# Optimization experiments

Measured on AMD Instinct MI355X. Metric: run time of the kernel, lower is better.

The kernel has to match this reference:

```python
import jax, jax.numpy as jnp
import numpy as np

B, S, D, H = 2, 2048, 1024, 16
DH = D // H  # per-head dim = 64


def setup_inputs() -> dict:
    key = jax.random.key(0)
    k0, k1, k2, k3, k4, k5 = jax.random.split(key, 6)
    x = jax.random.normal(k0, (B, S, D), dtype=jnp.float32)
    # mask: True where token is valid, False where padded ([B, S, 1] bool)
    mask = jax.random.randint(k1, (B, S, 1), 0, 2).astype(bool)
    scale = 0.02
    # Per-head projection weights stacked over heads: [H, D, DH]
    Wq = jax.random.normal(k2, (H, D, DH), dtype=jnp.float32) * scale
    Wk = jax.random.normal(k3, (H, D, DH), dtype=jnp.float32) * scale
    Wv = jax.random.normal(k4, (H, D, DH), dtype=jnp.float32) * scale
    # Output projection, torch Linear convention [out, in]: y = out @ Wo.T
    Wo = jax.random.normal(k5, (D, D), dtype=jnp.float32) * scale
    return {"x": x, "mask": mask, "Wq": Wq, "Wk": Wk, "Wv": Wv, "Wo": Wo}


def reference(x, mask, Wq, Wk, Wv, Wo):
    # Batched per-head projections (equivalent to the per-head Linear loop)
    q = jnp.einsum('bsd,hde->bhse', x, Wq)  # [B,H,S,DH]
    k = jnp.einsum('bsd,hde->bhse', x, Wk)
    v = jnp.einsum('bsd,hde->bhse', x, Wv)
    scale = 1.0 / np.sqrt(DH).astype(np.float32)
    scores = jnp.einsum('bhqe,bhke->bhqk', q, k) * scale  # [B,H,S,S]
    key_mask = mask[:, None, None, :, 0]   # [B,1,1,S]
    qry_mask = mask[:, None, :, :]          # [B,1,S,1]
    # masked keys get -1e10 added (same as original: +(~key_mask)*-1e10)
    scores = scores + (~key_mask) * jnp.float32(-1e10)
    attn = jax.nn.softmax(scores, axis=-1)
    attn = attn * qry_mask                  # zero rows for padded queries
    ctx = jnp.einsum('bhqk,bhke->bhqe', attn, v)  # [B,H,S,DH]
    # concat heads along last dim (head h -> contiguous slice, matches torch.cat)
    out = ctx.transpose(0, 2, 1, 3).reshape(B, S, D)
    return out @ Wo.T
```

## Files before the change

### kernel.cpp

```cpp
#include <hip/hip_runtime.h>
#include <hip/hip_bf16.h>

typedef __attribute__((ext_vector_type(8))) short sh8;
typedef __attribute__((ext_vector_type(4))) float f32x4;

#define LDC 136
#define QSCALE 0.18033688f
#define KMBF16 0xF14Au

#define EXP2F(x) __builtin_amdgcn_exp2f(x)

__device__ __forceinline__ void glds16(const unsigned short* g, unsigned short* l){
  __builtin_amdgcn_global_load_lds(
      (const __attribute__((address_space(1))) unsigned int*)g,
      (__attribute__((address_space(3))) unsigned int*)l, 16, 0, 0);
}

__device__ __forceinline__ unsigned short f2bf(float f){
  union { float f; unsigned u; } c; c.f = f;
  unsigned u = c.u;
  u += 0x7fffu + ((u >> 16) & 1u);
  return (unsigned short)(u >> 16);
}

__device__ __forceinline__ unsigned long long pack4bf(float a, float b, float c, float d){
  __hip_bfloat162 lo = __float22bfloat162_rn(make_float2(a, b));
  __hip_bfloat162 hi = __float22bfloat162_rn(make_float2(c, d));
  union { unsigned u[2]; unsigned long long ull; } pk;
  pk.u[0] = *(unsigned*)&lo; pk.u[1] = *(unsigned*)&hi;
  return pk.ull;
}

#define PREP_ZB   4096
#define PREP_CVT  5120
#define PREP_TR   768
__global__ __launch_bounds__(256) void prep(const float* __restrict__ x,
                                            const float* __restrict__ Wo,
                                            const float* __restrict__ Wq,
                                            const float* __restrict__ Wk,
                                            const float* __restrict__ Wv,
                                            const int* __restrict__ mask,
                                            unsigned short* __restrict__ x_bf,
                                            unsigned short* __restrict__ wo_bf,
                                            unsigned short* __restrict__ wt,
                                            unsigned short* __restrict__ kb_zero,
                                            int* __restrict__ pidx){
  __shared__ float tile[64][65];
  const int blk = blockIdx.x;
  const int t = threadIdx.x;

  if (blk < PREP_ZB){
    ((uint4*)kb_zero)[(size_t)blk*256 + t] = make_uint4(0,0,0,0);
    return;
  }
  if (blk < PREP_ZB + PREP_CVT){
    int i = (blk - PREP_ZB)*256 + t;
    const float* s; unsigned short* d;
    if (i < 1048576){ s = x; d = x_bf; }
    else { s = Wo; d = wo_bf; i -= 1048576; }
    float4 v = ((const float4*)s)[i];
    ushort4 o;
    o.x = f2bf(v.x); o.y = f2bf(v.y); o.z = f2bf(v.z); o.w = f2bf(v.w);
    ((ushort4*)d)[i] = o;
    return;
  }
  if (blk < PREP_ZB + PREP_CVT + PREP_TR){
    int idx = blk - (PREP_ZB + PREP_CVT);
    int jm = idx >> 8;
    int rest = idx & 255;
    int h = rest >> 4, dt = rest & 15;
    const float* src = (jm==0 ? Wq : (jm==1 ? Wk : Wv)) + (size_t)h*65536;
    {
      int r = t >> 2, c0 = (t & 3)*16;
      for (int i=0;i<4;++i){
        float4 v = *(const float4*)&src[(size_t)(dt*64 + r)*64 + c0 + i*4];
        tile[r][c0+i*4+0]=v.x; tile[r][c0+i*4+1]=v.y; tile[r][c0+i*4+2]=v.z; tile[r][c0+i*4+3]=v.w;
      }
    }
    __syncthreads();
    {
      int e = t >> 2, r0 = (t & 3)*16;
      int j = jm*1024 + h*64 + e;
      __align__(16) unsigned short buf[16];
      for (int i=0;i<16;++i) buf[i] = f2bf(tile[r0+i][e]);
      *(uint4*)&wt[(size_t)j*1024 + dt*64 + r0    ] = *(uint4*)&buf[0];
      *(uint4*)&wt[(size_t)j*1024 + dt*64 + r0 + 8] = *(uint4*)&buf[8];
    }
    return;
  }
  {
    int b = blk - (PREP_ZB + PREP_CVT + PREP_TR);
    if (t >= 64) return;
    int lane = t;
    int m[32];
    #pragma unroll
    for (int c = 0; c < 32; ++c) m[c] = mask[b*2048 + c*64 + lane];
    int base = 0;
    #pragma unroll
    for (int c = 0; c < 32; ++c){
      unsigned long long bal = __ballot(m[c] != 0);
      int pos = base + (int)__popcll(bal & ((1ULL << lane) - 1ULL));
      pidx[b*2048 + c*64 + lane] = m[c] ? pos : -1;
      base += (int)__popcll(bal);
    }
  }
}

template<int BM>
__global__ __launch_bounds__(256) void gemm_bt(const unsigned short* __restrict__ A,
                                               const unsigned short* __restrict__ Bt,
                                               unsigned short* __restrict__ Cq,
                                               unsigned short* __restrict__ Ck,
                                               unsigned short* __restrict__ Cv,
                                               float* __restrict__ Cf,
                                               const int* __restrict__ pidx,
                                               int M, int N, int K, int mode){
  constexpr int MI = BM/32;
  constexpr int ABUF = BM*64;
  constexpr int BBUF = 128*64;
  constexpr int BUFN = ABUF + BBUF;
  constexpr int TOTN = 2*BUFN;
  constexpr int SMEMN = (TOTN > 17664) ? TOTN : 17664;
  __shared__ __align__(16) unsigned short smem[SMEMN];
  const int t = threadIdx.x;
  const int w = t >> 6, lane = t & 63, l15 = lane & 15, quad = lane >> 4;

  int lin = blockIdx.y * gridDim.x + blockIdx.x;
  int gn = gridDim.x;
  int per = 8 * gn;
  int gid = lin / per, rem = lin % per;
  int j = rem / gn, nc = rem % gn;
  const int m0 = (gid*8 + j) * BM;
  const int n0 = nc * 128;

  const int wm = (w >> 1)*(BM/2), wn = (w & 1)*64;
  const int lr8 = lane >> 3;
  const int gc8 = (lane & 7) ^ lr8;
  const int h7 = l15 & 7;
  f32x4 acc[MI][4] = {};

  auto stage = [&](int k0, int bb){
    unsigned short* as = smem + bb*BUFN;
    unsigned short* bs = as + ABUF;
    for (int p = 0; p < BM/32; ++p){
      int rbase = p*32 + w*8;
      glds16(&A [(size_t)(m0 + rbase + lr8)*K + k0 + gc8*8], &as[rbase*64]);
    }
    for (int p = 0; p < 4; ++p){
      int rbase = p*32 + w*8;
      glds16(&Bt[(size_t)(n0 + rbase + lr8)*K + k0 + gc8*8], &bs[rbase*64]);
    }
  };

  const int NS = K >> 6;
  stage(0, 0);
  stage(64, 1);
  for (int ks = 0; ks < NS; ++ks){
    const int cb = ks & 1;
    if (ks == NS - 1){
      asm volatile("s_waitcnt vmcnt(0)" ::: "memory");
    } else {
      if constexpr (BM == 128) asm volatile("s_waitcnt vmcnt(8)" ::: "memory");
      else                     asm volatile("s_waitcnt vmcnt(6)" ::: "memory");
    }
    __builtin_amdgcn_s_barrier();
    __builtin_amdgcn_sched_barrier(0);

    const unsigned short* as = smem + cb*BUFN;
    const unsigned short* bs = as + ABUF;
    sh8 aF[2][MI], bF[2][4];
    #pragma unroll
    for (int kk = 0; kk < 2; ++kk){
      const int cs = (((kk<<2) + quad) ^ h7) * 8;
      for (int i = 0; i < MI; ++i)
        aF[kk][i] = *(const sh8*)&as[(wm + i*16 + l15)*64 + cs];
      for (int i = 0; i < 4; ++i)
        bF[kk][i] = *(const sh8*)&bs[(wn + i*16 + l15)*64 + cs];
    }
    asm volatile("s_waitcnt lgkmcnt(0)" ::: "memory");
    __builtin_amdgcn_sched_barrier(0);
    __builtin_amdgcn_s_barrier();
    __builtin_amdgcn_sched_barrier(0);
    if (ks + 2 < NS) stage((ks+2)*64, cb);

    #pragma unroll
    for (int kk = 0; kk < 2; ++kk)
      for (int mi = 0; mi < MI; ++mi)
        for (int ni = 0; ni < 4; ++ni)
          acc[mi][ni] = __builtin_amdgcn_mfma_f32_16x16x32_bf16(aF[kk][mi], bF[kk][ni], acc[mi][ni], 0, 0, 0);
  }

  if (mode == 2){
    for (int mi = 0; mi < MI; ++mi){
      int rowb = m0 + wm + mi*16 + quad*4;
      for (int ni = 0; ni < 4; ++ni){
        int col = n0 + wn + ni*16 + l15;
        for (int r = 0; r < 4; ++r)
          Cf[(size_t)(rowb + r)*N + col] = acc[mi][ni][r];
      }
    }
    return;
  }

  if constexpr (BM == 128){
    __syncthreads();
    unsigned short* Ct = smem;
    int* pS = (int*)(smem + 17408);
    const bool isv = (n0 >= 2048);
    const float cscale = (n0 < 1024) ? QSCALE : 1.0f;
    const int b = m0 >> 11, sbase = m0 & 2047;
    for (int mi = 0; mi < 4; ++mi){
      for (int ni = 0; ni < 4; ++ni){
        for (int r = 0; r < 4; ++r){
          int lr = wm + mi*16 + quad*4 + r;
          int lc = wn + ni*16 + l15;
          unsigned short bv = f2bf(acc[mi][ni][r] * cscale);
          if (isv) Ct[lc*LDC + lr] = bv;
          else     Ct[lr*LDC + lc] = bv;
        }
      }
    }
    if (t < 128) pS[t] = pidx[b*2048 + sbase + t];
    __syncthreads();

    const int hbase = (n0 & 1023) >> 6;
    if (!isv){
      const bool isq = (n0 < 1024);
      unsigned short* dst = isq ? Cq : Ck;
      for (int i = 0; i < 8; ++i){
        int s  = i*16 + (t >> 4);
        int hh = (t >> 3) & 1;
        int c  = t & 7;
        uint4 val = *(const uint4*)&Ct[s*LDC + hh*64 + c*8];
        int h = hbase + hh;
        int row;
        if (isq) row = sbase + s;
        else { int p = pS[s]; if (p < 0) continue; row = p; }
        *(uint4*)&dst[((size_t)(b*16 + h)*2048 + row)*64 + c*8] = val;
      }
    } else {
      for (int i = 0; i < 8; ++i){
        int ecol = i*16 + (t >> 4);
        int s0   = (t & 15)*8;
        int hh = ecol >> 6, e = ecol & 63;
        int h = hbase + hh;
        unsigned short* dr = &Cv[((size_t)(b*16 + h)*64 + e)*2048];
        union { uint4 v; unsigned short us[8]; } val;
        val.v = *(const uint4*)&Ct[ecol*LDC + s0];
        #pragma unroll
        for (int jj = 0; jj < 8; ++jj){
          int p = pS[s0 + jj];
          if (p >= 0) dr[p] = val.us[jj];
        }
      }
    }
  }
}

__global__ __launch_bounds__(512) void flash_attn(const unsigned short* __restrict__ q,
                                                  const unsigned short* __restrict__ k,
                                                  const unsigned short* __restrict__ vt,
                                                  const int* __restrict__ mask,
                                                  unsigned short* __restrict__ ctx){
  __shared__ __align__(16) unsigned short Ks[2][4096];
  __shared__ __align__(16) unsigned short Vs[2][4096];
  __shared__ __align__(16) unsigned short Ps[8][1024];
  __shared__ __align__(16) unsigned short kmb[2048];
  __shared__ int s_nv;

  const int idx = blockIdx.x;
  const int xcd = idx & 7, sub = idx >> 3;
  const int bh = xcd*4 + (sub & 3);
  const int qt = sub >> 2;
  const int b = bh >> 4, h = bh & 15;
  const int t = threadIdx.x;
  const int w = t >> 6, lane = t & 63, l15 = lane & 15, quad = lane >> 4;
  const size_t base = (size_t)bh * 2048 * 64;

  const unsigned short* qp0 = q + base + (size_t)(qt*128 + w*16 + l15)*64;
  sh8 qf[2];
  qf[0] = *(const sh8*)(qp0 +      quad*8);
  qf[1] = *(const sh8*)(qp0 + 32 + quad*8);

  if (t == 0) s_nv = 0;
  int4 mv = ((const int4*)(mask + b*2048))[t];
  __syncthreads();
  {
    int c = (mv.x != 0) + (mv.y != 0) + (mv.z != 0) + (mv.w != 0);
    c += __shfl_down(c, 32); c += __shfl_down(c, 16); c += __shfl_down(c, 8);
    c += __shfl_down(c, 4);  c += __shfl_down(c, 2);  c += __shfl_down(c, 1);
    if (lane == 0) atomicAdd(&s_nv, c);
  }
  __syncthreads();
  const int nv = s_nv;
  const int ntiles = (nv + 63) >> 6;

  {
    __align__(8) unsigned short tmp[4];
    #pragma unroll
    for (int i = 0; i < 4; ++i) tmp[i] = (t*4 + i < nv) ? 0 : (unsigned short)KMBF16;
    *(unsigned long long*)&kmb[t*4] = *(unsigned long long*)tmp;
  }

  const int lr8 = lane >> 3;
  const int gc8 = (lane & 7) ^ lr8;
  const int h7 = l15 & 7;
  const int cs0 = ((quad    ) ^ h7) * 8;
  const int cs1 = ((quad + 4) ^ h7) * 8;
  const int pw_off = (quad & 1)*4;
  const int pr0 = ((0*4 + quad) ^ h7) * 8;
  const int pr1 = ((1*4 + quad) ^ h7) * 8;

  auto stageKV = [&](int kt, int bb){
    int r0 = w*8;
    glds16(&k [base + (size_t)(kt*64 + r0 + lr8)*64 + gc8*8], &Ks[bb][r0*64]);
    glds16(&vt[base + (size_t)(r0 + lr8)*2048 + kt*64 + gc8*8], &Vs[bb][r0*64]);
  };

  float la[4] = {};
  f32x4 O[4] = {};

  if (ntiles > 0) stageKV(0, 0);
  for (int kt = 0; kt < ntiles; ++kt){
    const int bb = kt & 1;
    __syncthreads();
    if (kt + 1 < ntiles) stageKV(kt + 1, bb ^ 1);

    for (int mt = 0; mt < 4; ++mt){
      sh8 a0 = *(const sh8*)&Ks[bb][(mt*16 + l15)*64 + cs0];
      sh8 a1 = *(const sh8*)&Ks[bb][(mt*16 + l15)*64 + cs1];
      unsigned long long kq = *(const unsigned long long*)&kmb[kt*64 + mt*16 + quad*4];
      unsigned d0 = (unsigned)kq, d1 = (unsigned)(kq >> 32);
      f32x4 a;
      a[0] = __uint_as_float(d0 << 16);
      a[1] = __uint_as_float(d0 & 0xFFFF0000u);
      a[2] = __uint_as_float(d1 << 16);
      a[3] = __uint_as_float(d1 & 0xFFFF0000u);
      const int pwc = (((mt*2 + (quad>>1)) ^ h7) * 8) + pw_off;
      a = __builtin_amdgcn_mfma_f32_16x16x32_bf16(a0, qf[0], a, 0, 0, 0);
      a = __builtin_amdgcn_mfma_f32_16x16x32_bf16(a1, qf[1], a, 0, 0, 0);
      float e0 = EXP2F(a[0]); la[0] += e0;
      float e1 = EXP2F(a[1]); la[1] += e1;
      float e2 = EXP2F(a[2]); la[2] += e2;
      float e3 = EXP2F(a[3]); la[3] += e3;
      *(unsigned long long*)&Ps[w][l15*64 + pwc] = pack4bf(e0, e1, e2, e3);
    }

    sh8 pf0 = *(const sh8*)&Ps[w][l15*64 + pr0];
    sh8 pf1 = *(const sh8*)&Ps[w][l15*64 + pr1];
    for (int et = 0; et < 4; ++et){
      sh8 vf0 = *(const sh8*)&Vs[bb][(et*16 + l15)*64 + cs0];
      O[et] = __builtin_amdgcn_mfma_f32_16x16x32_bf16(vf0, pf0, O[et], 0, 0, 0);
    }
    for (int et = 0; et < 4; ++et){
      sh8 vf1 = *(const sh8*)&Vs[bb][(et*16 + l15)*64 + cs1];
      O[et] = __builtin_amdgcn_mfma_f32_16x16x32_bf16(vf1, pf1, O[et], 0, 0, 0);
    }
  }

  {
    float l_i = (la[0] + la[1]) + (la[2] + la[3]);
    l_i += __shfl_xor(l_i, 16);
    l_i += __shfl_xor(l_i, 32);
    int srow = qt*128 + w*16 + l15;
    bool qm = (mask[b*2048 + srow] != 0);
    float inv = (qm && l_i > 0.f) ? 1.f/l_i : 0.f;
    unsigned short* crow = ctx + (((size_t)b*2048 + srow)*16 + h)*64;
    for (int et = 0; et < 4; ++et)
      *(unsigned long long*)&crow[et*16 + quad*4] =
        pack4bf(O[et][0]*inv, O[et][1]*inv, O[et][2]*inv, O[et][3]*inv);
  }
}

extern "C" void kernel_launch(void* const* d_in, const int* in_sizes, int n_in,
                              void* d_out, int out_size, void* d_ws, size_t ws_size,
                              hipStream_t stream){
  const float* x  = (const float*)d_in[0];
  const int* mask = (const int*)  d_in[1];
  const float* Wq = (const float*)d_in[2];
  const float* Wk = (const float*)d_in[3];
  const float* Wv = (const float*)d_in[4];
  const float* Wo = (const float*)d_in[5];
  float* out = (float*)d_out;

  char* ws = (char*)d_ws;
  unsigned short* x_bf  = (unsigned short*)(ws);
  unsigned short* wt    = (unsigned short*)(ws + 8388608);
  unsigned short* wo_bf = (unsigned short*)(ws + 14680064);
  unsigned short* qb    = (unsigned short*)(ws + 16777216);
  unsigned short* kb    = (unsigned short*)(ws + 25165824);
  unsigned short* vtb   = (unsigned short*)(ws + 33554432);
  unsigned short* ctx   = (unsigned short*)(ws + 41943040);
  int*            pidx  = (int*)(ws + 41943040);

  prep<<<PREP_ZB + PREP_CVT + PREP_TR + 2, 256, 0, stream>>>(
      x, Wo, Wq, Wk, Wv, mask, x_bf, wo_bf, wt, kb, pidx);
  gemm_bt<128><<<dim3(24, 32), 256, 0, stream>>>(x_bf, wt, qb, kb, vtb, nullptr, pidx, 4096, 3072, 1024, 0);
  flash_attn<<<512, 512, 0, stream>>>(qb, kb, vtb, mask, ctx);
  gemm_bt<64><<<dim3(8, 64), 256, 0, stream>>>(ctx, wo_bf, nullptr, nullptr, nullptr, out, pidx, 4096, 1024, 1024, 2);
}
```

Measured before the change: 172.7 us.

## Gather valid rows before K/V projection and skip tiles past valid count

The prep kernel now builds a gather list of valid token indices per batch plus a valid count, in place of a scatter map. The QKV GEMM gathers valid rows of x for the K and V column blocks, so compacted K/V are computed directly, and whole tiles beyond the valid count exit early. Epilogue stores become contiguous (vectorized for V^T) instead of per-element scatter. This removes about half of the K/V projection work under a random mask, at the cost of indirect row addresses in the A loads.

Measured after the change: 172.1 us. About the same (-0.4%).

```diff
diff --git a/kernel.cpp b/kernel.cpp
--- a/kernel.cpp
+++ b/kernel.cpp
@@ -44,7 +44,8 @@
                                             unsigned short* __restrict__ wo_bf,
                                             unsigned short* __restrict__ wt,
                                             unsigned short* __restrict__ kb_zero,
-                                            int* __restrict__ pidx){
+                                            int* __restrict__ gidx,
+                                            int* __restrict__ nv){
   __shared__ float tile[64][65];
   const int blk = blockIdx.x;
   const int t = threadIdx.x;
@@ -95,14 +96,17 @@
     int m[32];
     #pragma unroll
     for (int c = 0; c < 32; ++c) m[c] = mask[b*2048 + c*64 + lane];
+    #pragma unroll
+    for (int c = 0; c < 32; ++c) gidx[b*2048 + c*64 + lane] = 0;
     int base = 0;
     #pragma unroll
     for (int c = 0; c < 32; ++c){
       unsigned long long bal = __ballot(m[c] != 0);
       int pos = base + (int)__popcll(bal & ((1ULL << lane) - 1ULL));
-      pidx[b*2048 + c*64 + lane] = m[c] ? pos : -1;
+      if (m[c]) gidx[b*2048 + pos] = c*64 + lane;
       base += (int)__popcll(bal);
     }
+    if (lane == 0) nv[b] = base;
   }
 }
 
@@ -113,14 +117,15 @@
                                                unsigned short* __restrict__ Ck,
                                                unsigned short* __restrict__ Cv,
                                                float* __restrict__ Cf,
-                                               const int* __restrict__ pidx,
+                                               const int* __restrict__ gidx,
+                                               const int* __restrict__ nv,
                                                int M, int N, int K, int mode){
   constexpr int MI = BM/32;
   constexpr int ABUF = BM*64;
   constexpr int BBUF = 128*64;
   constexpr int BUFN = ABUF + BBUF;
   constexpr int TOTN = 2*BUFN;
-  constexpr int SMEMN = (TOTN > 17664) ? TOTN : 17664;
+  constexpr int SMEMN = (TOTN > 17408) ? TOTN : 17408;
   __shared__ __align__(16) unsigned short smem[SMEMN];
   const int t = threadIdx.x;
   const int w = t >> 6, lane = t & 63, l15 = lane & 15, quad = lane >> 4;
@@ -137,6 +142,18 @@
   const int lr8 = lane >> 3;
   const int gc8 = (lane & 7) ^ lr8;
   const int h7 = l15 & 7;
+
+  const bool kvreg = (mode == 0) && (n0 >= 1024);
+  const int b_ = m0 >> 11, j0_ = m0 & 2047;
+  int nvb = 0;
+  int arow[MI];
+  if (kvreg){
+    nvb = nv[b_];
+    if (j0_ >= nvb) return;
+    #pragma unroll
+    for (int p = 0; p < MI; ++p)
+      arow[p] = b_*2048 + gidx[b_*2048 + j0_ + p*32 + w*8 + lr8];
+  }
   f32x4 acc[MI][4] = {};
 
   auto stage = [&](int k0, int bb){
@@ -144,7 +161,10 @@
     unsigned short* bs = as + ABUF;
     for (int p = 0; p < BM/32; ++p){
       int rbase = p*32 + w*8;
-      glds16(&A [(size_t)(m0 + rbase + lr8)*K + k0 + gc8*8], &as[rbase*64]);
+      const unsigned short* src = kvreg
+        ? &A[(size_t)arow[p]*K + k0 + gc8*8]
+        : &A[(size_t)(m0 + rbase + lr8)*K + k0 + gc8*8];
+      glds16(src, &as[rbase*64]);
     }
     for (int p = 0; p < 4; ++p){
       int rbase = p*32 + w*8;
@@ -205,10 +225,9 @@
   if constexpr (BM == 128){
     __syncthreads();
     unsigned short* Ct = smem;
-    int* pS = (int*)(smem + 17408);
     const bool isv = (n0 >= 2048);
-    const float cscale = (n0 < 1024) ? QSCALE : 1.0f;
-    const int b = m0 >> 11, sbase = m0 & 2047;
+    const bool isq = (n0 < 1024);
+    const float cscale = isq ? QSCALE : 1.0f;
     for (int mi = 0; mi < 4; ++mi){
       for (int ni = 0; ni < 4; ++ni){
         for (int r = 0; r < 4; ++r){
@@ -220,12 +239,10 @@
         }
       }
     }
-    if (t < 128) pS[t] = pidx[b*2048 + sbase + t];
     __syncthreads();
 
     const int hbase = (n0 & 1023) >> 6;
     if (!isv){
-      const bool isq = (n0 < 1024);
       unsigned short* dst = isq ? Cq : Ck;
       for (int i = 0; i < 8; ++i){
         int s  = i*16 + (t >> 4);
@@ -233,10 +250,9 @@
         int c  = t & 7;
         uint4 val = *(const uint4*)&Ct[s*LDC + hh*64 + c*8];
         int h = hbase + hh;
-        int row;
-        if (isq) row = sbase + s;
-        else { int p = pS[s]; if (p < 0) continue; row = p; }
-        *(uint4*)&dst[((size_t)(b*16 + h)*2048 + row)*64 + c*8] = val;
+        int row = j0_ + s;
+        if (!isq && row >= nvb) continue;
+        *(uint4*)&dst[((size_t)(b_*16 + h)*2048 + row)*64 + c*8] = val;
       }
     } else {
       for (int i = 0; i < 8; ++i){
@@ -244,13 +260,16 @@
         int s0   = (t & 15)*8;
         int hh = ecol >> 6, e = ecol & 63;
         int h = hbase + hh;
-        unsigned short* dr = &Cv[((size_t)(b*16 + h)*64 + e)*2048];
+        unsigned short* dr = &Cv[((size_t)(b_*16 + h)*64 + e)*2048];
         union { uint4 v; unsigned short us[8]; } val;
         val.v = *(const uint4*)&Ct[ecol*LDC + s0];
-        #pragma unroll
-        for (int jj = 0; jj < 8; ++jj){
-          int p = pS[s0 + jj];
-          if (p >= 0) dr[p] = val.us[jj];
+        int c0 = j0_ + s0;
+        if (c0 + 7 < nvb){
+          *(uint4*)&dr[c0] = val.v;
+        } else {
+          #pragma unroll
+          for (int jj = 0; jj < 8; ++jj)
+            if (c0 + jj < nvb) dr[c0 + jj] = val.us[jj];
         }
       }
     }
@@ -391,11 +410,12 @@
   unsigned short* kb    = (unsigned short*)(ws + 25165824);
   unsigned short* vtb   = (unsigned short*)(ws + 33554432);
   unsigned short* ctx   = (unsigned short*)(ws + 41943040);
-  int*            pidx  = (int*)(ws + 41943040);
+  int*            gidx  = (int*)(ws + 41943040);
+  int*            nvbuf = (int*)(ws + 41943040 + 16384);
 
   prep<<<PREP_ZB + PREP_CVT + PREP_TR + 2, 256, 0, stream>>>(
-      x, Wo, Wq, Wk, Wv, mask, x_bf, wo_bf, wt, kb, pidx);
-  gemm_bt<128><<<dim3(24, 32), 256, 0, stream>>>(x_bf, wt, qb, kb, vtb, nullptr, pidx, 4096, 3072, 1024, 0);
+      x, Wo, Wq, Wk, Wv, mask, x_bf, wo_bf, wt, kb, gidx, nvbuf);
+  gemm_bt<128><<<dim3(24, 32), 256, 0, stream>>>(x_bf, wt, qb, kb, vtb, nullptr, gidx, nvbuf, 4096, 3072, 1024, 0);
   flash_attn<<<512, 512, 0, stream>>>(qb, kb, vtb, mask, ctx);
-  gemm_bt<64><<<dim3(8, 64), 256, 0, stream>>>(ctx, wo_bf, nullptr, nullptr, nullptr, out, pidx, 4096, 1024, 1024, 2);
-}
+  gemm_bt<64><<<dim3(8, 64), 256, 0, stream>>>(ctx, wo_bf, nullptr, nullptr, nullptr, out, nullptr, nullptr, 4096, 1024, 1024, 2);
+}
```

## Switch GEMM mainloop to triple-buffered K=32 stages with single barrier

Applied to the files above, without the earlier changes.

Replaces the double-buffered 64-wide K stages in the GEMM with three 32-wide LDS buffers and a new swizzle for loads and fragment reads. The next stage is prefetched right after the barrier, so the second barrier and lgkmcnt wait per iteration go away and loads overlap compute over a deeper pipeline. The cost is twice as many loop iterations and barriers, and only one MFMA k-step per barrier, which gives less compute to hide latency behind. The output projection call also passes a null pidx, which is harmless in mode 2.

Measured after the change: 171.2 us. Within noise of the previous version (-0.9%).

```diff
diff --git a/kernel.cpp b/kernel.cpp
--- a/kernel.cpp
+++ b/kernel.cpp
@@ -116,10 +116,10 @@
                                                const int* __restrict__ pidx,
                                                int M, int N, int K, int mode){
   constexpr int MI = BM/32;
-  constexpr int ABUF = BM*64;
-  constexpr int BBUF = 128*64;
+  constexpr int ABUF = BM*32;
+  constexpr int BBUF = 128*32;
   constexpr int BUFN = ABUF + BBUF;
-  constexpr int TOTN = 2*BUFN;
+  constexpr int TOTN = 3*BUFN;
   constexpr int SMEMN = (TOTN > 17664) ? TOTN : 17664;
   __shared__ __align__(16) unsigned short smem[SMEMN];
   const int t = threadIdx.x;
@@ -134,60 +134,52 @@
   const int n0 = nc * 128;
 
   const int wm = (w >> 1)*(BM/2), wn = (w & 1)*64;
-  const int lr8 = lane >> 3;
-  const int gc8 = (lane & 7) ^ lr8;
-  const int h7 = l15 & 7;
+  const int lr16 = lane >> 2;
+  const int gq   = ((lane & 3) - (lane >> 3)) & 3;
+  const int cs   = ((quad + (l15 >> 1)) & 3) * 8;
   f32x4 acc[MI][4] = {};
 
   auto stage = [&](int k0, int bb){
     unsigned short* as = smem + bb*BUFN;
     unsigned short* bs = as + ABUF;
-    for (int p = 0; p < BM/32; ++p){
-      int rbase = p*32 + w*8;
-      glds16(&A [(size_t)(m0 + rbase + lr8)*K + k0 + gc8*8], &as[rbase*64]);
-    }
-    for (int p = 0; p < 4; ++p){
-      int rbase = p*32 + w*8;
-      glds16(&Bt[(size_t)(n0 + rbase + lr8)*K + k0 + gc8*8], &bs[rbase*64]);
+    for (int p = 0; p < BM/64; ++p){
+      int r0 = w*(BM/4) + p*16;
+      glds16(&A [(size_t)(m0 + r0 + lr16)*K + k0 + gq*8], &as[r0*32]);
+    }
+    for (int p = 0; p < 2; ++p){
+      int r0 = w*32 + p*16;
+      glds16(&Bt[(size_t)(n0 + r0 + lr16)*K + k0 + gq*8], &bs[r0*32]);
     }
   };
 
-  const int NS = K >> 6;
+  const int NS = K >> 5;
   stage(0, 0);
-  stage(64, 1);
+  stage(32, 1);
+  int cb = 0, sb = 2;
   for (int ks = 0; ks < NS; ++ks){
-    const int cb = ks & 1;
     if (ks == NS - 1){
       asm volatile("s_waitcnt vmcnt(0)" ::: "memory");
     } else {
-      if constexpr (BM == 128) asm volatile("s_waitcnt vmcnt(8)" ::: "memory");
-      else                     asm volatile("s_waitcnt vmcnt(6)" ::: "memory");
+      if constexpr (BM == 128) asm volatile("s_waitcnt vmcnt(4)" ::: "memory");
+      else                     asm volatile("s_waitcnt vmcnt(3)" ::: "memory");
     }
     __builtin_amdgcn_s_barrier();
     __builtin_amdgcn_sched_barrier(0);
+    if (ks + 2 < NS) stage((ks+2)*32, sb);
 
     const unsigned short* as = smem + cb*BUFN;
     const unsigned short* bs = as + ABUF;
-    sh8 aF[2][MI], bF[2][4];
-    #pragma unroll
-    for (int kk = 0; kk < 2; ++kk){
-      const int cs = (((kk<<2) + quad) ^ h7) * 8;
-      for (int i = 0; i < MI; ++i)
-        aF[kk][i] = *(const sh8*)&as[(wm + i*16 + l15)*64 + cs];
-      for (int i = 0; i < 4; ++i)
-        bF[kk][i] = *(const sh8*)&bs[(wn + i*16 + l15)*64 + cs];
-    }
-    asm volatile("s_waitcnt lgkmcnt(0)" ::: "memory");
-    __builtin_amdgcn_sched_barrier(0);
-    __builtin_amdgcn_s_barrier();
-    __builtin_amdgcn_sched_barrier(0);
-    if (ks + 2 < NS) stage((ks+2)*64, cb);
-
-    #pragma unroll
-    for (int kk = 0; kk < 2; ++kk)
-      for (int mi = 0; mi < MI; ++mi)
-        for (int ni = 0; ni < 4; ++ni)
-          acc[mi][ni] = __builtin_amdgcn_mfma_f32_16x16x32_bf16(aF[kk][mi], bF[kk][ni], acc[mi][ni], 0, 0, 0);
+    sh8 aF[MI], bF[4];
+    for (int i = 0; i < MI; ++i)
+      aF[i] = *(const sh8*)&as[(wm + i*16 + l15)*32 + cs];
+    for (int i = 0; i < 4; ++i)
+      bF[i] = *(const sh8*)&bs[(wn + i*16 + l15)*32 + cs];
+    for (int mi = 0; mi < MI; ++mi)
+      for (int ni = 0; ni < 4; ++ni)
+        acc[mi][ni] = __builtin_amdgcn_mfma_f32_16x16x32_bf16(aF[mi], bF[ni], acc[mi][ni], 0, 0, 0);
+
+    cb = (cb == 2) ? 0 : cb + 1;
+    sb = (sb == 2) ? 0 : sb + 1;
   }
 
   if (mode == 2){
@@ -397,5 +389,5 @@
       x, Wo, Wq, Wk, Wv, mask, x_bf, wo_bf, wt, kb, pidx);
   gemm_bt<128><<<dim3(24, 32), 256, 0, stream>>>(x_bf, wt, qb, kb, vtb, nullptr, pidx, 4096, 3072, 1024, 0);
   flash_attn<<<512, 512, 0, stream>>>(qb, kb, vtb, mask, ctx);
-  gemm_bt<64><<<dim3(8, 64), 256, 0, stream>>>(ctx, wo_bf, nullptr, nullptr, nullptr, out, pidx, 4096, 1024, 1024, 2);
-}
+  gemm_bt<64><<<dim3(8, 64), 256, 0, stream>>>(ctx, wo_bf, nullptr, nullptr, nullptr, out, nullptr, 4096, 1024, 1024, 2);
+}
```
